# Kernel optimization log

Measured on AMD Instinct MI355X. Metric: run time of the kernel, lower is better.

Reference implementation:

```python
import jax, jax.numpy as jnp
import numpy as np

N_NODES = 102
EDGES = [[0,6],[0,5],[6,8],[5,7],[0,31],[31,32],[32,33],[28,33],[28,29],[29,30],[30,31],[0,43],[40,41],[41,42],[42,43],[43,44],[44,45],[45,46],[46,47],[47,48],[48,49],[49,50],[50,51],[40,51],[40,52],[46,56],[52,53],[53,54],[54,55],[55,56],[56,57],[57,58],[58,59],[52,59],[0,34],[34,35],[35,36],[36,37],[37,38],[38,39],[34,39],[7,60],[60,61],[61,62],[62,63],[63,64],[60,65],[65,66],[66,67],[67,68],[60,69],[69,70],[70,71],[71,72],[60,73],[73,74],[74,75],[75,76],[60,77],[77,78],[78,79],[79,80],[8,81],[81,82],[82,83],[83,84],[84,85],[81,86],[86,87],[87,88],[88,89],[81,90],[90,91],[91,92],[92,93],[81,94],[94,95],[95,96],[96,97],[81,98],[98,99],[99,100],[100,101]]


def _gcn_norm_adj(edge_index):
    # PyG GCNConv: add self-loops, symmetric normalization.
    # deg computed over target (col) index including self-loops.
    row, col = edge_index[0], edge_index[1]
    deg = jnp.zeros((N_NODES,), jnp.float32).at[col].add(1.0) + 1.0  # +1 for self-loop
    dinv = jnp.where(deg > 0, 1.0 / jnp.sqrt(deg), 0.0)
    norm = dinv[row] * dinv[col]
    # out[col] += norm * x[row]  ->  A[col, row] = norm; self-loops on diagonal.
    A = jnp.zeros((N_NODES, N_NODES), jnp.float32).at[col, row].add(norm)
    A = A + jnp.diag(dinv * dinv)
    return A


def setup_inputs() -> dict:
    key = jax.random.key(0)
    k1, k2, k3, k4, k5 = jax.random.split(key, 5)
    B, n = 32, 256
    hidden, embed = 256, 256
    x = jax.random.normal(k1, (B, n, N_NODES * 2), jnp.float32)
    W_gnn = jax.random.normal(k2, (2, hidden), jnp.float32) * 0.5
    b_gnn = jax.random.normal(k3, (hidden,), jnp.float32) * 0.1
    W_proj = jax.random.normal(k4, (hidden, embed), jnp.float32) * (1.0 / np.sqrt(hidden))
    b_proj = jax.random.normal(k5, (embed,), jnp.float32) * 0.1
    edge_index = jnp.asarray(np.array(EDGES, dtype=np.int32).T)  # [2, 84]
    return {"x": x, "W_gnn": W_gnn, "b_gnn": b_gnn,
            "W_proj": W_proj, "b_proj": b_proj, "edge_index": edge_index}


def reference(x, W_gnn, b_gnn, W_proj, b_proj, edge_index):
    B, n, _ = x.shape
    xf = x.reshape(B, n, N_NODES, 2)                      # [B, n, 102, 2]
    A = _gcn_norm_adj(edge_index)                         # [102, 102]
    xw = jnp.einsum('bnuc,ch->bnuh', xf, W_gnn)           # transform
    h = jnp.einsum('vu,bnuh->bnvh', A, xw) + b_gnn        # propagate + bias
    h = jax.nn.relu(h)
    out = jnp.einsum('bnvh,he->bnve', h, W_proj) + b_proj # [B, n, 102, embed]
    return out
```

## Files before the change

### kernel.cpp

```cpp
#include <hip/hip_runtime.h>

#define N_NODES 102
#define NP 8192
#define RBLOCKS 3264
#define RSTRIDE 128

typedef _Float16 f16x8 __attribute__((ext_vector_type(8)));
typedef _Float16 f16x2 __attribute__((ext_vector_type(2)));
typedef float f32x4 __attribute__((ext_vector_type(4)));

__global__ void build_tables(const int* __restrict__ ei, int ne,
                             int4* __restrict__ gtu, float4* __restrict__ gtw) {
    __shared__ int   deg[N_NODES];
    __shared__ float dinv[N_NODES];
    __shared__ int   cnt[N_NODES];
    __shared__ int   tu[N_NODES][4];
    __shared__ float tw[N_NODES][4];
    int t = threadIdx.x;
    if (t < N_NODES) deg[t] = 1;
    __syncthreads();
    if (t == 0) for (int e = 0; e < ne; ++e) deg[ei[ne + e]] += 1;
    __syncthreads();
    if (t < N_NODES) {
        dinv[t] = 1.0f / sqrtf((float)deg[t]);
        cnt[t] = 1;
        for (int j = 0; j < 4; ++j) { tu[t][j] = 2 * t; tw[t][j] = 0.0f; }
    }
    __syncthreads();
    if (t < N_NODES) tw[t][0] = dinv[t] * dinv[t];
    __syncthreads();
    if (t == 0) {
        for (int e = 0; e < ne; ++e) {
            int r = ei[e], c = ei[ne + e];
            int s = cnt[c] < 4 ? cnt[c] : 3;
            cnt[c] = s + 1;
            tu[c][s] = 2 * r;
            tw[c][s] = dinv[r] * dinv[c];
        }
    }
    __syncthreads();
    if (t < N_NODES) {
        gtu[t] = make_int4(tu[t][0], tu[t][1], tu[t][2], tu[t][3]);
        gtw[t] = make_float4(tw[t][0], tw[t][1], tw[t][2], tw[t][3]);
    }
}

__global__ void prep_w(const float* __restrict__ Wp, _Float16* __restrict__ WpT) {
    int tid = blockIdx.x * 256 + threadIdx.x;
    for (int i = tid; i < 65536; i += 16384) {
        int col = i & 255, k = i >> 8;
        WpT[col * 256 + k] = (_Float16)Wp[i];
    }
}

__global__ __launch_bounds__(256, 2) void gnn_main(
    const float* __restrict__ x,
    const _Float16* __restrict__ WpT,
    const int4*  __restrict__ gtu,
    const float4* __restrict__ gtw,
    const float* __restrict__ Wg,
    const float* __restrict__ bg,
    const float* __restrict__ bp,
    float* __restrict__ out)
{
    __shared__ float xs[4 * 2 * N_NODES];
    __shared__ int4   stu[N_NODES];
    __shared__ float4 stw[N_NODES];
    __shared__ _Float16 W0l[256], W1l[256], bgl[256];
    const int tid = threadIdx.x;
    const int w  = tid >> 6;
    const int l  = tid & 63;
    const int qk = l >> 4;
    const int m  = l & 15;
    const int c0  = blockIdx.y * 64;
    const int rbi = blockIdx.x;

    f16x8 bfragR[8][4];
    #pragma unroll
    for (int t = 0; t < 8; ++t)
        #pragma unroll
        for (int nt = 0; nt < 4; ++nt)
            bfragR[t][nt] = *reinterpret_cast<const f16x8*>(
                &WpT[(c0 + nt * 16 + m) * 256 + qk * 8 + 32 * t]);

    if (tid < N_NODES) { stu[tid] = gtu[tid]; stw[tid] = gtw[tid]; }
    W0l[tid] = (_Float16)Wg[tid];
    W1l[tid] = (_Float16)Wg[256 + tid];
    bgl[tid] = (_Float16)bg[tid];

    float bpf[4];
    #pragma unroll
    for (int nt = 0; nt < 4; ++nt) bpf[nt] = bp[c0 + nt * 16 + m];

    const f16x2 z2 = (f16x2){ (_Float16)0.0f, (_Float16)0.0f };

    #pragma unroll 1
    for (int j = 0; j < 26; ++j) {
        const int rb = rbi + j * RSTRIDE;
        if (rb >= RBLOCKS) break;
        const int rowblk = rb * 256;
        const int pbase  = rowblk / N_NODES;

        __syncthreads();
        #pragma unroll
        for (int pi = 0; pi < 4; ++pi) {
            int p = pbase + pi;
            if (tid < 2 * N_NODES)
                xs[pi * 2 * N_NODES + tid] = (p < NP) ? x[(size_t)p * (2 * N_NODES) + tid] : 0.0f;
        }
        __syncthreads();

        f16x2 y0pk[4], y1pk[4];
        #pragma unroll
        for (int s = 0; s < 4; ++s) {
            int r = rowblk + w * 64 + s * 16 + m;
            int p = r / N_NODES;
            int v = r - p * N_NODES;
            const float* xp = &xs[(p - pbase) * 2 * N_NODES];
            int4  U = stu[v];
            float4 W = stw[v];
            float a0 = W.x * xp[U.x]     + W.y * xp[U.y]
                     + W.z * xp[U.z]     + W.w * xp[U.w];
            float a1 = W.x * xp[U.x + 1] + W.y * xp[U.y + 1]
                     + W.z * xp[U.z + 1] + W.w * xp[U.w + 1];
            _Float16 h0 = (_Float16)a0;
            _Float16 h1 = (_Float16)a1;
            y0pk[s] = (f16x2){ h0, h0 };
            y1pk[s] = (f16x2){ h1, h1 };
        }

        const long rowbase = (long)rowblk + (long)w * 64;

        #pragma unroll
        for (int s = 0; s < 4; ++s) {
            f32x4 acc[4];
            #pragma unroll
            for (int nt = 0; nt < 4; ++nt) acc[nt] = (f32x4){0.f, 0.f, 0.f, 0.f};

            #pragma unroll
            for (int t = 0; t < 8; ++t) {
                const int kk = qk * 8 + 32 * t;
                union { f16x8 v; f16x2 p[4]; } w0u, w1u, bbu;
                w0u.v = *reinterpret_cast<const f16x8*>(&W0l[kk]);
                w1u.v = *reinterpret_cast<const f16x8*>(&W1l[kk]);
                bbu.v = *reinterpret_cast<const f16x8*>(&bgl[kk]);
                union { f16x8 v; f16x2 p[4]; } af;
                #pragma unroll
                for (int j2 = 0; j2 < 4; ++j2) {
                    f16x2 h = w0u.p[j2] * y0pk[s] + w1u.p[j2] * y1pk[s] + bbu.p[j2];
                    af.p[j2] = __builtin_elementwise_max(h, z2);
                }
                #pragma unroll
                for (int nt = 0; nt < 4; ++nt)
                    acc[nt] = __builtin_amdgcn_mfma_f32_16x16x32_f16(af.v, bfragR[t][nt], acc[nt], 0, 0, 0);
            }

            #pragma unroll
            for (int nt = 0; nt < 4; ++nt) {
                const int e = c0 + nt * 16 + m;
                #pragma unroll
                for (int reg = 0; reg < 4; ++reg) {
                    long r = rowbase + s * 16 + qk * 4 + reg;
                    out[r * 256 + e] = acc[nt][reg] + bpf[nt];
                }
            }
        }
    }
}

extern "C" void kernel_launch(void* const* d_in, const int* in_sizes, int n_in,
                              void* d_out, int out_size, void* d_ws, size_t ws_size,
                              hipStream_t stream) {
    const float* x  = (const float*)d_in[0];
    const float* Wg = (const float*)d_in[1];
    const float* bg = (const float*)d_in[2];
    const float* Wp = (const float*)d_in[3];
    const float* bp = (const float*)d_in[4];
    const int* ei   = (const int*)d_in[5];
    float* out = (float*)d_out;

    const int ne = in_sizes[5] / 2;

    int4*     gtu = (int4*)d_ws;
    float4*   gtw = (float4*)((char*)d_ws + 2048);
    _Float16* WpT = (_Float16*)((char*)d_ws + 4096);

    build_tables<<<1, 128, 0, stream>>>(ei, ne, gtu, gtw);
    prep_w<<<64, 256, 0, stream>>>(Wp, WpT);

    gnn_main<<<dim3(RSTRIDE, 4), 256, 0, stream>>>(x, WpT, gtu, gtw, Wg, bg, bp, out);
}
```

Before: 236.2 us.

## Precompute graph propagation in separate kernel and register-prefetch it in main loop

New measurement: 218.7 us. -7.4%, faster.

```diff
diff --git a/kernel.cpp b/kernel.cpp
--- a/kernel.cpp
+++ b/kernel.cpp
@@ -2,6 +2,7 @@
 
 #define N_NODES 102
 #define NP 8192
+#define NROWS 835584
 #define RBLOCKS 3264
 #define RSTRIDE 128
 
@@ -53,19 +54,88 @@
     }
 }
 
+__global__ void compute_y(const float* __restrict__ x,
+                          const int4* __restrict__ gtu,
+                          const float4* __restrict__ gtw,
+                          float2* __restrict__ y) {
+    int r = blockIdx.x * 256 + threadIdx.x;
+    int p = r / N_NODES;
+    int v = r - p * N_NODES;
+    int4  U = gtu[v];
+    float4 W = gtw[v];
+    const float* xp = x + (size_t)p * (2 * N_NODES);
+    float a0 = W.x * xp[U.x]     + W.y * xp[U.y]
+             + W.z * xp[U.z]     + W.w * xp[U.w];
+    float a1 = W.x * xp[U.x + 1] + W.y * xp[U.y + 1]
+             + W.z * xp[U.z + 1] + W.w * xp[U.w + 1];
+    y[r] = make_float2(a0, a1);
+}
+
+#define GNN_BODY(YC, YN, ROWBLK, PREF_OK, PREF_RB)                                   \
+    {                                                                                \
+        const int rowblk_ = (ROWBLK);                                                \
+        f16x2 y0pk[4], y1pk[4];                                                      \
+        _Pragma("unroll")                                                            \
+        for (int s = 0; s < 4; ++s) {                                                \
+            _Float16 h0 = (_Float16)YC[s].x;                                         \
+            _Float16 h1 = (_Float16)YC[s].y;                                         \
+            y0pk[s] = (f16x2){ h0, h0 };                                             \
+            y1pk[s] = (f16x2){ h1, h1 };                                             \
+        }                                                                            \
+        if (PREF_OK) {                                                               \
+            const long rbase_ = (long)(PREF_RB) * 256 + w * 64 + m;                  \
+            _Pragma("unroll")                                                        \
+            for (int s = 0; s < 4; ++s) YN[s] = yg[rbase_ + s * 16];                 \
+        }                                                                            \
+        f32x4 acc[4][4];                                                             \
+        _Pragma("unroll")                                                            \
+        for (int s = 0; s < 4; ++s)                                                  \
+            _Pragma("unroll")                                                        \
+            for (int nt = 0; nt < 4; ++nt) acc[s][nt] = (f32x4){0.f,0.f,0.f,0.f};    \
+        _Pragma("unroll")                                                            \
+        for (int t = 0; t < 8; ++t) {                                                \
+            const int kk = qk * 8 + 32 * t;                                          \
+            union { f16x8 v; f16x2 p[4]; } w0u, w1u, bbu;                            \
+            w0u.v = *reinterpret_cast<const f16x8*>(&W0l[kk]);                       \
+            w1u.v = *reinterpret_cast<const f16x8*>(&W1l[kk]);                       \
+            bbu.v = *reinterpret_cast<const f16x8*>(&bgl[kk]);                       \
+            _Pragma("unroll")                                                        \
+            for (int s = 0; s < 4; ++s) {                                            \
+                union { f16x8 v; f16x2 p[4]; } af;                                   \
+                _Pragma("unroll")                                                    \
+                for (int j2 = 0; j2 < 4; ++j2) {                                     \
+                    f16x2 h = w0u.p[j2] * y0pk[s] + w1u.p[j2] * y1pk[s] + bbu.p[j2]; \
+                    af.p[j2] = __builtin_elementwise_max(h, z2);                     \
+                }                                                                    \
+                _Pragma("unroll")                                                    \
+                for (int nt = 0; nt < 4; ++nt)                                       \
+                    acc[s][nt] = __builtin_amdgcn_mfma_f32_16x16x32_f16(             \
+                        af.v, bfragR[t][nt], acc[s][nt], 0, 0, 0);                   \
+            }                                                                        \
+        }                                                                            \
+        const long rowbase_ = (long)rowblk_ + (long)w * 64;                          \
+        _Pragma("unroll")                                                            \
+        for (int s = 0; s < 4; ++s) {                                                \
+            _Pragma("unroll")                                                        \
+            for (int nt = 0; nt < 4; ++nt) {                                         \
+                const int e = c0 + nt * 16 + m;                                      \
+                _Pragma("unroll")                                                    \
+                for (int reg = 0; reg < 4; ++reg) {                                  \
+                    long r = rowbase_ + s * 16 + qk * 4 + reg;                       \
+                    out[r * 256 + e] = acc[s][nt][reg] + bpf[nt];                    \
+                }                                                                    \
+            }                                                                        \
+        }                                                                            \
+    }
+
 __global__ __launch_bounds__(256, 2) void gnn_main(
-    const float* __restrict__ x,
+    const float2* __restrict__ yg,
     const _Float16* __restrict__ WpT,
-    const int4*  __restrict__ gtu,
-    const float4* __restrict__ gtw,
     const float* __restrict__ Wg,
     const float* __restrict__ bg,
     const float* __restrict__ bp,
     float* __restrict__ out)
 {
-    __shared__ float xs[4 * 2 * N_NODES];
-    __shared__ int4   stu[N_NODES];
-    __shared__ float4 stw[N_NODES];
     __shared__ _Float16 W0l[256], W1l[256], bgl[256];
     const int tid = threadIdx.x;
     const int w  = tid >> 6;
@@ -83,7 +153,6 @@
             bfragR[t][nt] = *reinterpret_cast<const f16x8*>(
                 &WpT[(c0 + nt * 16 + m) * 256 + qk * 8 + 32 * t]);
 
-    if (tid < N_NODES) { stu[tid] = gtu[tid]; stw[tid] = gtw[tid]; }
     W0l[tid] = (_Float16)Wg[tid];
     W1l[tid] = (_Float16)Wg[256 + tid];
     bgl[tid] = (_Float16)bg[tid];
@@ -92,78 +161,27 @@
     #pragma unroll
     for (int nt = 0; nt < 4; ++nt) bpf[nt] = bp[c0 + nt * 16 + m];
 
+    float2 yA[4], yB[4];
+    {
+        const long rbase = (long)rbi * 256 + w * 64 + m;
+        #pragma unroll
+        for (int s = 0; s < 4; ++s) yA[s] = yg[rbase + s * 16];
+    }
+    __syncthreads();
+
     const f16x2 z2 = (f16x2){ (_Float16)0.0f, (_Float16)0.0f };
 
     #pragma unroll 1
-    for (int j = 0; j < 26; ++j) {
-        const int rb = rbi + j * RSTRIDE;
-        if (rb >= RBLOCKS) break;
-        const int rowblk = rb * 256;
-        const int pbase  = rowblk / N_NODES;
-
-        __syncthreads();
-        #pragma unroll
-        for (int pi = 0; pi < 4; ++pi) {
-            int p = pbase + pi;
-            if (tid < 2 * N_NODES)
-                xs[pi * 2 * N_NODES + tid] = (p < NP) ? x[(size_t)p * (2 * N_NODES) + tid] : 0.0f;
-        }
-        __syncthreads();
-
-        f16x2 y0pk[4], y1pk[4];
-        #pragma unroll
-        for (int s = 0; s < 4; ++s) {
-            int r = rowblk + w * 64 + s * 16 + m;
-            int p = r / N_NODES;
-            int v = r - p * N_NODES;
-            const float* xp = &xs[(p - pbase) * 2 * N_NODES];
-            int4  U = stu[v];
-            float4 W = stw[v];
-            float a0 = W.x * xp[U.x]     + W.y * xp[U.y]
-                     + W.z * xp[U.z]     + W.w * xp[U.w];
-            float a1 = W.x * xp[U.x + 1] + W.y * xp[U.y + 1]
-                     + W.z * xp[U.z + 1] + W.w * xp[U.w + 1];
-            _Float16 h0 = (_Float16)a0;
-            _Float16 h1 = (_Float16)a1;
-            y0pk[s] = (f16x2){ h0, h0 };
-            y1pk[s] = (f16x2){ h1, h1 };
-        }
-
-        const long rowbase = (long)rowblk + (long)w * 64;
-
-        #pragma unroll
-        for (int s = 0; s < 4; ++s) {
-            f32x4 acc[4];
-            #pragma unroll
-            for (int nt = 0; nt < 4; ++nt) acc[nt] = (f32x4){0.f, 0.f, 0.f, 0.f};
-
-            #pragma unroll
-            for (int t = 0; t < 8; ++t) {
-                const int kk = qk * 8 + 32 * t;
-                union { f16x8 v; f16x2 p[4]; } w0u, w1u, bbu;
-                w0u.v = *reinterpret_cast<const f16x8*>(&W0l[kk]);
-                w1u.v = *reinterpret_cast<const f16x8*>(&W1l[kk]);
-                bbu.v = *reinterpret_cast<const f16x8*>(&bgl[kk]);
-                union { f16x8 v; f16x2 p[4]; } af;
-                #pragma unroll
-                for (int j2 = 0; j2 < 4; ++j2) {
-                    f16x2 h = w0u.p[j2] * y0pk[s] + w1u.p[j2] * y1pk[s] + bbu.p[j2];
-                    af.p[j2] = __builtin_elementwise_max(h, z2);
-                }
-                #pragma unroll
-                for (int nt = 0; nt < 4; ++nt)
-                    acc[nt] = __builtin_amdgcn_mfma_f32_16x16x32_f16(af.v, bfragR[t][nt], acc[nt], 0, 0, 0);
-            }
-
-            #pragma unroll
-            for (int nt = 0; nt < 4; ++nt) {
-                const int e = c0 + nt * 16 + m;
-                #pragma unroll
-                for (int reg = 0; reg < 4; ++reg) {
-                    long r = rowbase + s * 16 + qk * 4 + reg;
-                    out[r * 256 + e] = acc[nt][reg] + bpf[nt];
-                }
-            }
+    for (int jj = 0; jj < 13; ++jj) {
+        const int jA = 2 * jj, jB = 2 * jj + 1;
+        const int rbA = rbi + jA * RSTRIDE;
+        const int rbB = rbi + jB * RSTRIDE;
+        const int rbN = rbi + (jA + 2) * RSTRIDE;
+
+        GNN_BODY(yA, yB, rbA * 256, (rbB < RBLOCKS), rbB)
+
+        if (rbB < RBLOCKS) {
+            GNN_BODY(yB, yA, rbB * 256, (rbN < RBLOCKS), rbN)
         }
     }
 }
@@ -184,9 +202,11 @@
     int4*     gtu = (int4*)d_ws;
     float4*   gtw = (float4*)((char*)d_ws + 2048);
     _Float16* WpT = (_Float16*)((char*)d_ws + 4096);
+    float2*   yws = (float2*)((char*)d_ws + 4096 + 131072);
 
     build_tables<<<1, 128, 0, stream>>>(ei, ne, gtu, gtw);
     prep_w<<<64, 256, 0, stream>>>(Wp, WpT);
-
-    gnn_main<<<dim3(RSTRIDE, 4), 256, 0, stream>>>(x, WpT, gtu, gtw, Wg, bg, bp, out);
-}
+    compute_y<<<NROWS / 256, 256, 0, stream>>>(x, gtu, gtw, yws);
+
+    gnn_main<<<dim3(RSTRIDE, 4), 256, 0, stream>>>(yws, WpT, Wg, bg, bp, out);
+}
```
